# Optimization experiments

Hardware: AMD Instinct MI355X
Metric: run time of the kernel (lower is better)

The kernel has to match this reference:

```python
import jax, jax.numpy as jnp
import numpy as np
import math

D_MODEL = 768
N_HEADS = 12
B, L = 2, 2048
ALPHA = 0.3

def setup_inputs() -> dict:
    key = jax.random.key(0)
    ks = jax.random.split(key, 7)
    s = 0.02
    return {
        "x": jax.random.normal(ks[0], (B, L, D_MODEL), dtype=jnp.float32),
        "Wqkv_w": jax.random.normal(ks[1], (D_MODEL, 3 * D_MODEL), dtype=jnp.float32) * s,
        "Wqkv_b": jax.random.normal(ks[2], (3 * D_MODEL,), dtype=jnp.float32) * s,
        "sel_w": jax.random.normal(ks[3], (D_MODEL, 2), dtype=jnp.float32) * s,
        "sel_b": jax.random.normal(ks[4], (2,), dtype=jnp.float32) * s,
        "out_w": jax.random.normal(ks[5], (D_MODEL, D_MODEL), dtype=jnp.float32) * s,
        "out_b": jax.random.normal(ks[6], (D_MODEL,), dtype=jnp.float32) * s,
        "temperature": jnp.ones((1,), dtype=jnp.float32) * (math.sqrt(D_MODEL) * ALPHA),
    }

def reference(x, Wqkv_w, Wqkv_b, sel_w, sel_b, out_w, out_b, temperature):
    b, l, d = x.shape
    h = N_HEADS
    hd = d // h
    # QKV projection: (B, L, 3, H, hd)
    qkv = (x @ Wqkv_w + Wqkv_b).reshape(b, l, 3, h, hd)
    q, k_, v = qkv[:, :, 0], qkv[:, :, 1], qkv[:, :, 2]
    scale = 1.0 / math.sqrt(hd)
    scores = jnp.einsum('bthd,bshd->bhts', q, k_ * scale)  # (B,H,L,L)
    causal_mask = jnp.triu(jnp.full((l, l), -10000.0, dtype=scores.dtype), 1)
    attn = jax.nn.softmax(scores + causal_mask, axis=-1)
    ctx = jnp.einsum('bhts,bshd->bthd', attn, v).reshape(b, l, d)
    attn_output = ctx @ out_w + out_b  # (B,L,D)
    # selection gate: softmax over 2 logits, keep prob of class 1 -> (B,L,1)
    selection = jax.nn.softmax((x @ sel_w + sel_b) / temperature, axis=-1)[..., 1:]
    # eval-mode top-k routing
    k_sel = int(math.ceil(math.sqrt(l)))
    _, idx = jax.lax.top_k(selection[..., 0], k_sel)  # (B, k)
    gated = attn_output * selection  # (B,L,D)
    src = jnp.take_along_axis(gated, idx[..., None], axis=1)  # (B,k,D)
    y = jax.vmap(lambda xb, ib, sb: xb.at[ib].add(sb))(x, idx, src)
    return y
```

## Files before the change

### kernel.cpp

```cpp
#include <hip/hip_runtime.h>
#include <hip/hip_bf16.h>
#include <cstddef>

#define BATCH 2
#define SEQ   2048
#define DM    768
#define NH    12
#define HD    64
#define N3    2304
#define NKV   1536
#define KSEL  46
#define NROW  (BATCH*KSEL)
#define NCHUNK 32

typedef unsigned short ushort_t;
typedef __attribute__((ext_vector_type(8))) short bf16x8;
typedef __attribute__((ext_vector_type(4))) float f32x4;

__device__ __forceinline__ ushort_t f2bf(float f) {
  union { __hip_bfloat16 h; ushort_t u; } cv;
  cv.h = __float2bfloat16(f);
  return cv.u;
}
__device__ __forceinline__ float bf2f(ushort_t u) {
  union { unsigned int i; float f; } cv;
  cv.i = ((unsigned int)u) << 16;
  return cv.f;
}

#define GLD16(g, l)                                                         \
  __builtin_amdgcn_global_load_lds(                                         \
      (const __attribute__((address_space(1))) void*)(g),                   \
      (__attribute__((address_space(3))) void*)(l), 16, 0, 0)

__global__ __launch_bounds__(256) void prep_kernel(
    const float* __restrict__ x, const float* __restrict__ W,
    const float* __restrict__ Wo,
    const float* __restrict__ sel_w, const float* __restrict__ sel_b,
    const float* __restrict__ temp,
    ushort_t* __restrict__ xb, ushort_t* __restrict__ Wt,
    ushort_t* __restrict__ WoT,
    float* __restrict__ sel, float* __restrict__ y) {
  const int bx = blockIdx.x;
  const int tid = threadIdx.x;
  if (bx < 3072) {
    int i = bx * 256 + tid;
    float4 f = ((const float4*)x)[i];
    ushort4 o;
    o.x = f2bf(f.x); o.y = f2bf(f.y); o.z = f2bf(f.z); o.w = f2bf(f.w);
    ((ushort4*)xb)[i] = o;
  } else if (bx < 4800) {
    __shared__ float tile[32][33];
    const int bx2 = bx - 3072;
    const int n0 = (bx2 % 72) * 32, k0 = (bx2 / 72) * 32;
    const int r = tid >> 3, c4 = (tid & 7) * 4;
    float4 f = *(const float4*)&W[(size_t)(k0 + r) * N3 + n0 + c4];
    tile[r][c4] = f.x; tile[r][c4 + 1] = f.y; tile[r][c4 + 2] = f.z; tile[r][c4 + 3] = f.w;
    __syncthreads();
    ushort4 o;
    o.x = f2bf(tile[c4 + 0][r]);
    o.y = f2bf(tile[c4 + 1][r]);
    o.z = f2bf(tile[c4 + 2][r]);
    o.w = f2bf(tile[c4 + 3][r]);
    *(ushort4*)&Wt[(size_t)(n0 + r) * DM + k0 + c4] = o;
  } else if (bx < 5376) {
    __shared__ float tile2[32][33];
    const int bx3 = bx - 4800;
    const int n0 = (bx3 % 24) * 32, k0 = (bx3 / 24) * 32;
    const int r = tid >> 3, c4 = (tid & 7) * 4;
    float4 f = *(const float4*)&Wo[(size_t)(k0 + r) * DM + n0 + c4];
    tile2[r][c4] = f.x; tile2[r][c4 + 1] = f.y; tile2[r][c4 + 2] = f.z; tile2[r][c4 + 3] = f.w;
    __syncthreads();
    ushort4 o;
    o.x = f2bf(tile2[c4 + 0][r]);
    o.y = f2bf(tile2[c4 + 1][r]);
    o.z = f2bf(tile2[c4 + 2][r]);
    o.w = f2bf(tile2[c4 + 3][r]);
    *(ushort4*)&WoT[(size_t)(n0 + r) * DM + k0 + c4] = o;
  } else if (bx < 6400) {
    int wave = tid >> 6, lane = tid & 63;
    int row = (bx - 5376) * 4 + wave;
    const float* xr = x + (size_t)row * DM;
    float a0 = 0.f, a1 = 0.f;
    for (int i = 0; i < DM / 64; ++i) {
      int k = lane + 64 * i;
      float xv = xr[k];
      a0 += xv * sel_w[2 * k];
      a1 += xv * sel_w[2 * k + 1];
    }
    for (int off = 32; off; off >>= 1) {
      a0 += __shfl_xor(a0, off);
      a1 += __shfl_xor(a1, off);
    }
    if (lane == 0) {
      float t = temp[0];
      float l0 = (a0 + sel_b[0]) / t;
      float l1 = (a1 + sel_b[1]) / t;
      sel[row] = 1.0f / (1.0f + expf(l0 - l1));
    }
  } else {
    int i = (bx - 6400) * 256 + tid;
    ((float4*)y)[i] = ((const float4*)x)[i];
  }
}

__global__ __launch_bounds__(256) void topk_kernel(
    const float* __restrict__ sel, int* __restrict__ idx,
    int* __restrict__ idxp) {
  __shared__ unsigned int hist[256];
  __shared__ unsigned int cum[256];
  __shared__ int sh_b;
  __shared__ int c_gt, c_eq;
  __shared__ int tmp_gt[KSEL];
  __shared__ int eqlist[256];
  const int b = blockIdx.x, tid = threadIdx.x;

  unsigned int key[8];
  int  kidx[8];
#pragma unroll
  for (int e = 0; e < 8; ++e) {
    int i = e * 256 + tid;
    kidx[e] = i;
    key[e] = __float_as_uint(sel[b * SEQ + i]);
  }
  unsigned int prefix = 0, mask = 0;
  int r = KSEL;
#pragma unroll
  for (int p = 3; p >= 0; --p) {
    const int shift = 8 * p;
    hist[tid] = 0;
    __syncthreads();
#pragma unroll
    for (int e = 0; e < 8; ++e)
      if ((key[e] & mask) == prefix)
        atomicAdd(&hist[(key[e] >> shift) & 255], 1u);
    __syncthreads();
    cum[tid] = hist[tid];
    __syncthreads();
    for (int d = 1; d < 256; d <<= 1) {
      unsigned int t = (tid + d < 256) ? cum[tid + d] : 0;
      __syncthreads();
      cum[tid] += t;
      __syncthreads();
    }
    if (cum[tid] >= (unsigned int)r && (tid == 255 || cum[tid + 1] < (unsigned int)r))
      sh_b = tid;
    __syncthreads();
    const int bsel = sh_b;
    r -= (bsel == 255) ? 0 : (int)cum[bsel + 1];
    prefix |= ((unsigned int)bsel) << shift;
    mask |= 0xFFu << shift;
    __syncthreads();
  }
  if (tid == 0) { c_gt = 0; c_eq = 0; }
  __syncthreads();
#pragma unroll
  for (int e = 0; e < 8; ++e) {
    if (key[e] > prefix) {
      int pos = atomicAdd(&c_gt, 1);
      tmp_gt[pos] = kidx[e];
    } else if (key[e] == prefix) {
      int pos = atomicAdd(&c_eq, 1);
      if (pos < 256) eqlist[pos] = kidx[e];
    }
  }
  __syncthreads();
  if (tid == 0) {
    const int need = KSEL - c_gt;
    const int ec = (c_eq < 256) ? c_eq : 256;
    for (int a = 0; a < need; ++a) {
      int mb = a;
      for (int bb = a + 1; bb < ec; ++bb)
        if (eqlist[bb] < eqlist[mb]) mb = bb;
      int tv = eqlist[a]; eqlist[a] = eqlist[mb]; eqlist[mb] = tv;
    }
  }
  __syncthreads();
  if (tid < 64) {
    if (tid < KSEL) {
      int t = (tid < c_gt) ? tmp_gt[tid] : eqlist[tid - c_gt];
      idx[b * KSEL + tid] = t;
      idxp[b * 64 + tid] = t;
    } else {
      idxp[b * 64 + tid] = 0;
    }
  }
}

__global__ __launch_bounds__(256) void gemm_kernel(
    const ushort_t* __restrict__ Xbf,
    const ushort_t* __restrict__ Wt,
    const float* __restrict__ bias,
    const int* __restrict__ idxp,
    ushort_t* __restrict__ Ckv,
    ushort_t* __restrict__ qb) {
  __shared__ ushort_t As[128 * 32];
  __shared__ ushort_t Bs[128 * 32];
  const int bid = blockIdx.x;
  const int tid = threadIdx.x;
  const int lane = tid & 63, w = tid >> 6;
  const int wr = w >> 1, wc = w & 1;
  const int quad = lane >> 4, l16 = lane & 15;
  const int ci0 = tid;
  const int ci1 = 256 + tid;
  const bool isQ = (bid >= 384);
  int m0, n0;
  size_t ga0, ga1;
  if (isQ) {
    m0 = 0;
    n0 = (bid - 384) * 128;
    const int r0 = ci0 >> 2, r1 = ci1 >> 2;
    ga0 = (size_t)((r0 >> 6) * SEQ + idxp[r0]) * DM;
    ga1 = (size_t)((r1 >> 6) * SEQ + idxp[r1]) * DM;
  } else {
    m0 = (bid / 12) * 128;
    n0 = 768 + (bid % 12) * 128;
    ga0 = (size_t)(m0 + (ci0 >> 2)) * DM;
    ga1 = (size_t)(m0 + (ci1 >> 2)) * DM;
  }
  const size_t gb0 = (size_t)(n0 + (ci0 >> 2)) * DM;
  const size_t gb1 = (size_t)(n0 + (ci1 >> 2)) * DM;
  const int ka0 = (ci0 & 3) * 8, ka1 = (ci1 & 3) * 8;

  f32x4 acc[4][4] = {};
  for (int k0 = 0; k0 < DM; k0 += 32) {
    GLD16(Xbf + ga0 + k0 + ka0, &As[(w * 64) * 8]);
    GLD16(Xbf + ga1 + k0 + ka1, &As[(256 + w * 64) * 8]);
    GLD16(Wt + gb0 + k0 + ka0, &Bs[(w * 64) * 8]);
    GLD16(Wt + gb1 + k0 + ka1, &Bs[(256 + w * 64) * 8]);
    __syncthreads();
    bf16x8 af[4], bfr[4];
#pragma unroll
    for (int i = 0; i < 4; ++i)
      af[i] = *(const bf16x8*)&As[(wr * 64 + i * 16 + l16) * 32 + quad * 8];
#pragma unroll
    for (int j = 0; j < 4; ++j)
      bfr[j] = *(const bf16x8*)&Bs[(wc * 64 + j * 16 + l16) * 32 + quad * 8];
#pragma unroll
    for (int i = 0; i < 4; ++i)
#pragma unroll
      for (int j = 0; j < 4; ++j)
        acc[i][j] = __builtin_amdgcn_mfma_f32_16x16x32_bf16(af[i], bfr[j], acc[i][j], 0, 0, 0);
    __syncthreads();
  }
#pragma unroll
  for (int i = 0; i < 4; ++i) {
    const int row_base = wr * 64 + i * 16 + quad * 4;
#pragma unroll
    for (int j = 0; j < 4; ++j) {
      const int col = n0 + wc * 64 + j * 16 + l16;
      const float bv = bias[col];
      if (isQ) {
#pragma unroll
        for (int r = 0; r < 4; ++r)
          qb[(size_t)(row_base + r) * DM + col] = f2bf(acc[i][j][r] + bv);
      } else {
#pragma unroll
        for (int r = 0; r < 4; ++r)
          Ckv[(size_t)(m0 + row_base + r) * NKV + (col - 768)] = f2bf(acc[i][j][r] + bv);
      }
    }
  }
}

__global__ __launch_bounds__(256) void attn_chunk_kernel(
    const ushort_t* __restrict__ kv,
    const ushort_t* __restrict__ qb,
    const int* __restrict__ idx,
    float* __restrict__ m_part, float* __restrict__ l_part,
    ushort_t* __restrict__ o_part) {
  __shared__ __align__(16) ushort_t Vt[64][72];
  __shared__ __align__(16) ushort_t Ps[4][16][72];
  __shared__ int tS[64];
  __shared__ int tmaxS;
  const int tid = threadIdx.x;
  const int c = blockIdx.x, h = blockIdx.y, b = blockIdx.z;
  const int c0 = c * 64;
  if (tid < 64) {
    int t = (tid < KSEL) ? idx[b * KSEL + tid] : -1;
    tS[tid] = t;
    int tm = t;
    for (int off = 32; off; off >>= 1) tm = max(tm, __shfl_xor(tm, off));
    if (tid == 0) tmaxS = tm;
  }
  __syncthreads();
  if (c0 > tmaxS) return;

  {
    const int key = tid >> 2, ds0 = (tid & 3) * 16;
    const ushort_t* vsrc = kv + (size_t)(b * SEQ + c0 + key) * NKV + DM + h * HD + ds0;
    ushort_t tmp[16];
    *(uint4*)&tmp[0] = *(const uint4*)&vsrc[0];
    *(uint4*)&tmp[8] = *(const uint4*)&vsrc[8];
#pragma unroll
    for (int i = 0; i < 16; ++i) Vt[ds0 + i][key] = tmp[i];
  }

  const int lane = tid & 63, w = tid >> 6;
  const int quad = lane >> 4, l16 = lane & 15;

  const ushort_t* qsrc = qb + (size_t)(b * 64 + w * 16 + l16) * DM + h * HD + quad * 8;
  bf16x8 aq0 = *(const bf16x8*)&qsrc[0];
  bf16x8 aq1 = *(const bf16x8*)&qsrc[32];

  f32x4 acc[4] = {};
#pragma unroll
  for (int nt = 0; nt < 4; ++nt) {
    const ushort_t* ksrc = kv + (size_t)(b * SEQ + c0 + nt * 16 + l16) * NKV + h * HD + quad * 8;
    bf16x8 bk0 = *(const bf16x8*)&ksrc[0];
    bf16x8 bk1 = *(const bf16x8*)&ksrc[32];
    acc[nt] = __builtin_amdgcn_mfma_f32_16x16x32_bf16(aq0, bk0, acc[nt], 0, 0, 0);
    acc[nt] = __builtin_amdgcn_mfma_f32_16x16x32_bf16(aq1, bk1, acc[nt], 0, 0, 0);
  }

  float p[4][4];
  float mrow[4], lrow[4];
#pragma unroll
  for (int r = 0; r < 4; ++r) {
    const int q = w * 16 + quad * 4 + r;
    const int t = tS[q];
    float mx = -1e30f;
#pragma unroll
    for (int nt = 0; nt < 4; ++nt) {
      float s = acc[nt][r] * 0.125f;
      if (c0 + nt * 16 + l16 > t) s = -1e30f;
      p[nt][r] = s;
      mx = fmaxf(mx, s);
    }
#pragma unroll
    for (int off = 1; off < 16; off <<= 1) mx = fmaxf(mx, __shfl_xor(mx, off));
    float sum = 0.f;
#pragma unroll
    for (int nt = 0; nt < 4; ++nt) {
      float pv = __expf(p[nt][r] - mx);
      p[nt][r] = pv;
      sum += pv;
    }
#pragma unroll
    for (int off = 1; off < 16; off <<= 1) sum += __shfl_xor(sum, off);
    mrow[r] = mx; lrow[r] = sum;
  }

  const size_t pbase = ((size_t)(b * NH + h) * NCHUNK + c) * 64;
  if (l16 == 0) {
#pragma unroll
    for (int r = 0; r < 4; ++r) {
      const int q = w * 16 + quad * 4 + r;
      m_part[pbase + q] = mrow[r];
      l_part[pbase + q] = lrow[r];
    }
  }

#pragma unroll
  for (int r = 0; r < 4; ++r)
#pragma unroll
    for (int nt = 0; nt < 4; ++nt)
      Ps[w][quad * 4 + r][nt * 16 + l16] = f2bf(p[nt][r]);
  __syncthreads();

  bf16x8 ap0 = *(const bf16x8*)&Ps[w][l16][quad * 8];
  bf16x8 ap1 = *(const bf16x8*)&Ps[w][l16][32 + quad * 8];
  f32x4 acc2[4] = {};
#pragma unroll
  for (int nt = 0; nt < 4; ++nt) {
    bf16x8 bv0 = *(const bf16x8*)&Vt[nt * 16 + l16][quad * 8];
    bf16x8 bv1 = *(const bf16x8*)&Vt[nt * 16 + l16][32 + quad * 8];
    acc2[nt] = __builtin_amdgcn_mfma_f32_16x16x32_bf16(ap0, bv0, acc2[nt], 0, 0, 0);
    acc2[nt] = __builtin_amdgcn_mfma_f32_16x16x32_bf16(ap1, bv1, acc2[nt], 0, 0, 0);
  }
  ushort_t* obp = o_part + pbase * 64;
#pragma unroll
  for (int nt = 0; nt < 4; ++nt)
#pragma unroll
    for (int r = 0; r < 4; ++r)
      obp[(w * 16 + quad * 4 + r) * 64 + nt * 16 + l16] = f2bf(acc2[nt][r]);
}

__global__ __launch_bounds__(256) void attn_combine_kernel(
    const float* __restrict__ m_part, const float* __restrict__ l_part,
    const ushort_t* __restrict__ o_part, const int* __restrict__ idx,
    ushort_t* __restrict__ ctx_bf) {
  __shared__ float wgt[NCHUNK][16];
  __shared__ float linv[16];
  __shared__ int ncS[16];
  const int rg = blockIdx.x, h = blockIdx.y, b = blockIdx.z;
  const int tid = threadIdx.x;
  const size_t base = (size_t)(b * NH + h) * NCHUNK * 64;
  if (tid < 16) {
    const int q = rg * 16 + tid;
    float L = 0.f; int nc = 0;
    if (q < KSEL) {
      const int t = idx[b * KSEL + q];
      nc = (t >> 6) + 1;
      float M = -1e30f;
      for (int cc = 0; cc < nc; ++cc)
        M = fmaxf(M, m_part[base + cc * 64 + q]);
      for (int cc = 0; cc < nc; ++cc) {
        float wv = __expf(m_part[base + cc * 64 + q] - M);
        wgt[cc][tid] = wv;
        L += wv * l_part[base + cc * 64 + q];
      }
    }
    ncS[tid] = nc;
    linv[tid] = (L > 0.f) ? 1.0f / L : 0.f;
  }
  __syncthreads();
  const int rl = tid >> 4;
  const int d4 = (tid & 15) * 4;
  const int q = rg * 16 + rl;
  if (q >= KSEL) return;
  const int nc = ncS[rl];
  float4 a = {0.f, 0.f, 0.f, 0.f};
  const ushort_t* obp = o_part + base * 64 + (size_t)q * 64 + d4;
  for (int cc = 0; cc < nc; ++cc) {
    const float wv = wgt[cc][rl];
    const ushort4 ov = *(const ushort4*)&obp[(size_t)cc * 4096];
    a.x += wv * bf2f(ov.x); a.y += wv * bf2f(ov.y);
    a.z += wv * bf2f(ov.z); a.w += wv * bf2f(ov.w);
  }
  const float li = linv[rl];
  ushort4 o;
  o.x = f2bf(a.x * li); o.y = f2bf(a.y * li);
  o.z = f2bf(a.z * li); o.w = f2bf(a.w * li);
  *(ushort4*)&ctx_bf[(size_t)(b * 64 + q) * DM + h * HD + d4] = o;
}

__global__ __launch_bounds__(256) void outproj_kernel(
    const ushort_t* __restrict__ ctx_bf,
    const ushort_t* __restrict__ WoT,
    const float* __restrict__ ob, const int* __restrict__ idx,
    const float* __restrict__ sel, float* __restrict__ y) {
  __shared__ ushort_t As[128 * 32];
  __shared__ ushort_t Bs[128 * 32];
  const int tid = threadIdx.x;
  const int lane = tid & 63, w = tid >> 6;
  const int wr = w >> 1, wc = w & 1;
  const int n0 = blockIdx.x * 128;
  const int quad = lane >> 4, l16 = lane & 15;
  const int ci0 = tid;
  const int ci1 = 256 + tid;
  const size_t ga0 = (size_t)(ci0 >> 2) * DM;
  const size_t ga1 = (size_t)(ci1 >> 2) * DM;
  const size_t gb0 = (size_t)(n0 + (ci0 >> 2)) * DM;
  const size_t gb1 = (size_t)(n0 + (ci1 >> 2)) * DM;
  const int ka0 = (ci0 & 3) * 8, ka1 = (ci1 & 3) * 8;
  f32x4 acc[4][4] = {};
  for (int k0 = 0; k0 < DM; k0 += 32) {
    GLD16(ctx_bf + ga0 + k0 + ka0, &As[(w * 64) * 8]);
    GLD16(ctx_bf + ga1 + k0 + ka1, &As[(256 + w * 64) * 8]);
    GLD16(WoT + gb0 + k0 + ka0, &Bs[(w * 64) * 8]);
    GLD16(WoT + gb1 + k0 + ka1, &Bs[(256 + w * 64) * 8]);
    __syncthreads();
    bf16x8 af[4], bfr[4];
#pragma unroll
    for (int i = 0; i < 4; ++i)
      af[i] = *(const bf16x8*)&As[(wr * 64 + i * 16 + l16) * 32 + quad * 8];
#pragma unroll
    for (int j = 0; j < 4; ++j)
      bfr[j] = *(const bf16x8*)&Bs[(wc * 64 + j * 16 + l16) * 32 + quad * 8];
#pragma unroll
    for (int i = 0; i < 4; ++i)
#pragma unroll
      for (int j = 0; j < 4; ++j)
        acc[i][j] = __builtin_amdgcn_mfma_f32_16x16x32_bf16(af[i], bfr[j], acc[i][j], 0, 0, 0);
    __syncthreads();
  }
#pragma unroll
  for (int i = 0; i < 4; ++i) {
#pragma unroll
    for (int r = 0; r < 4; ++r) {
      const int row = wr * 64 + i * 16 + quad * 4 + r;
      const int b = row >> 6, jj = row & 63;
      if (jj >= KSEL) continue;
      const int t = idx[b * KSEL + jj];
      const float sv = sel[b * SEQ + t];
      float* yr = y + (size_t)(b * SEQ + t) * DM;
#pragma unroll
      for (int j = 0; j < 4; ++j) {
        const int col = n0 + wc * 64 + j * 16 + l16;
        yr[col] += (acc[i][j][r] + ob[col]) * sv;
      }
    }
  }
}

extern "C" void kernel_launch(void* const* d_in, const int* in_sizes, int n_in,
                              void* d_out, int out_size, void* d_ws, size_t ws_size,
                              hipStream_t stream) {
  const float* x      = (const float*)d_in[0];
  const float* Wqkv_w = (const float*)d_in[1];
  const float* Wqkv_b = (const float*)d_in[2];
  const float* sel_w  = (const float*)d_in[3];
  const float* sel_b  = (const float*)d_in[4];
  const float* out_w  = (const float*)d_in[5];
  const float* out_b  = (const float*)d_in[6];
  const float* temp   = (const float*)d_in[7];
  float* y = (float*)d_out;

  char* wsb = (char*)d_ws;
  ushort_t* kv     = (ushort_t*)wsb;  wsb += (size_t)BATCH * SEQ * NKV * 2;
  ushort_t* o_part = (ushort_t*)wsb;  wsb += (size_t)24 * NCHUNK * 64 * 64 * 2;
  float*    m_part = (float*)wsb;     wsb += (size_t)24 * NCHUNK * 64 * 4;
  float*    l_part = (float*)wsb;     wsb += (size_t)24 * NCHUNK * 64 * 4;
  float*    sel    = (float*)wsb;     wsb += (size_t)BATCH * SEQ * 4;
  int*      idx    = (int*)wsb;       wsb += 128 * 4;
  int*      idxp   = (int*)wsb;       wsb += 128 * 4;
  ushort_t* ctx_bf = (ushort_t*)wsb;  wsb += (size_t)128 * DM * 2;
  ushort_t* qb     = (ushort_t*)wsb;  wsb += (size_t)128 * DM * 2;
  ushort_t* Xbf    = (ushort_t*)wsb;  wsb += (size_t)BATCH * SEQ * DM * 2;
  ushort_t* Wt     = (ushort_t*)wsb;  wsb += (size_t)N3 * DM * 2;
  ushort_t* WoT    = (ushort_t*)wsb;  wsb += (size_t)DM * DM * 2;

  prep_kernel<<<dim3(9472), 256, 0, stream>>>(x, Wqkv_w, out_w, sel_w, sel_b, temp,
                                              Xbf, Wt, WoT, sel, y);
  topk_kernel<<<dim3(BATCH), 256, 0, stream>>>(sel, idx, idxp);
  gemm_kernel<<<dim3(390), 256, 0, stream>>>(Xbf, Wt, Wqkv_b, idxp, kv, qb);
  attn_chunk_kernel<<<dim3(NCHUNK, NH, BATCH), 256, 0, stream>>>(kv, qb, idx, m_part, l_part, o_part);
  attn_combine_kernel<<<dim3(3, NH, BATCH), 256, 0, stream>>>(m_part, l_part, o_part, idx, ctx_bf);
  outproj_kernel<<<dim3(6), 256, 0, stream>>>(ctx_bf, WoT, out_b, idx, sel, y);
}
```

Measured before the change: 160.4 us.

## Fuse prep passes, sort top-k indices descending, skip inactive attention waves, split-K outproj

Merges the x-to-bf16 conversion, the copy of x into y and the selection-gate dot product into one pass per row, so x is read once instead of three times. Top-k indices are now sorted in descending position order. The attention chunk kernel can then exit early by comparing against the first index, and it skips whole waves whose queries all precede the chunk. The output projection is split in two along K across 12 blocks and accumulates with atomics, adding parallelism at the cost of atomic traffic and nondeterministic float summation order.

```diff
diff --git a/kernel.cpp b/kernel.cpp
--- a/kernel.cpp
+++ b/kernel.cpp
@@ -43,15 +43,39 @@
     float* __restrict__ sel, float* __restrict__ y) {
   const int bx = blockIdx.x;
   const int tid = threadIdx.x;
-  if (bx < 3072) {
-    int i = bx * 256 + tid;
-    float4 f = ((const float4*)x)[i];
-    ushort4 o;
-    o.x = f2bf(f.x); o.y = f2bf(f.y); o.z = f2bf(f.z); o.w = f2bf(f.w);
-    ((ushort4*)xb)[i] = o;
-  } else if (bx < 4800) {
+  if (bx < 4096) {
+    __shared__ float s0[4], s1[4];
+    const int r = bx;
+    const int wv = tid >> 6, lane = tid & 63;
+    float a0 = 0.f, a1 = 0.f;
+    if (tid < 192) {
+      const int i = r * 192 + tid;
+      const float4 f = ((const float4*)x)[i];
+      ((float4*)y)[i] = f;
+      ushort4 o;
+      o.x = f2bf(f.x); o.y = f2bf(f.y); o.z = f2bf(f.z); o.w = f2bf(f.w);
+      ((ushort4*)xb)[i] = o;
+      const int k = tid * 4;
+      a0 = f.x * sel_w[2*k] + f.y * sel_w[2*k+2] + f.z * sel_w[2*k+4] + f.w * sel_w[2*k+6];
+      a1 = f.x * sel_w[2*k+1] + f.y * sel_w[2*k+3] + f.z * sel_w[2*k+5] + f.w * sel_w[2*k+7];
+    }
+    for (int off = 32; off; off >>= 1) {
+      a0 += __shfl_xor(a0, off);
+      a1 += __shfl_xor(a1, off);
+    }
+    if (lane == 0) { s0[wv] = a0; s1[wv] = a1; }
+    __syncthreads();
+    if (tid == 0) {
+      float b0 = s0[0] + s0[1] + s0[2] + s0[3];
+      float b1 = s1[0] + s1[1] + s1[2] + s1[3];
+      float t = temp[0];
+      float l0 = (b0 + sel_b[0]) / t;
+      float l1 = (b1 + sel_b[1]) / t;
+      sel[r] = 1.0f / (1.0f + expf(l0 - l1));
+    }
+  } else if (bx < 5824) {
     __shared__ float tile[32][33];
-    const int bx2 = bx - 3072;
+    const int bx2 = bx - 4096;
     const int n0 = (bx2 % 72) * 32, k0 = (bx2 / 72) * 32;
     const int r = tid >> 3, c4 = (tid & 7) * 4;
     float4 f = *(const float4*)&W[(size_t)(k0 + r) * N3 + n0 + c4];
@@ -63,9 +87,9 @@
     o.z = f2bf(tile[c4 + 2][r]);
     o.w = f2bf(tile[c4 + 3][r]);
     *(ushort4*)&Wt[(size_t)(n0 + r) * DM + k0 + c4] = o;
-  } else if (bx < 5376) {
+  } else {
     __shared__ float tile2[32][33];
-    const int bx3 = bx - 4800;
+    const int bx3 = bx - 5824;
     const int n0 = (bx3 % 24) * 32, k0 = (bx3 / 24) * 32;
     const int r = tid >> 3, c4 = (tid & 7) * 4;
     float4 f = *(const float4*)&Wo[(size_t)(k0 + r) * DM + n0 + c4];
@@ -77,30 +101,6 @@
     o.z = f2bf(tile2[c4 + 2][r]);
     o.w = f2bf(tile2[c4 + 3][r]);
     *(ushort4*)&WoT[(size_t)(n0 + r) * DM + k0 + c4] = o;
-  } else if (bx < 6400) {
-    int wave = tid >> 6, lane = tid & 63;
-    int row = (bx - 5376) * 4 + wave;
-    const float* xr = x + (size_t)row * DM;
-    float a0 = 0.f, a1 = 0.f;
-    for (int i = 0; i < DM / 64; ++i) {
-      int k = lane + 64 * i;
-      float xv = xr[k];
-      a0 += xv * sel_w[2 * k];
-      a1 += xv * sel_w[2 * k + 1];
-    }
-    for (int off = 32; off; off >>= 1) {
-      a0 += __shfl_xor(a0, off);
-      a1 += __shfl_xor(a1, off);
-    }
-    if (lane == 0) {
-      float t = temp[0];
-      float l0 = (a0 + sel_b[0]) / t;
-      float l1 = (a1 + sel_b[1]) / t;
-      sel[row] = 1.0f / (1.0f + expf(l0 - l1));
-    }
-  } else {
-    int i = (bx - 6400) * 256 + tid;
-    ((float4*)y)[i] = ((const float4*)x)[i];
   }
 }
 
@@ -113,6 +113,7 @@
   __shared__ int c_gt, c_eq;
   __shared__ int tmp_gt[KSEL];
   __shared__ int eqlist[256];
+  __shared__ int win[KSEL];
   const int b = blockIdx.x, tid = threadIdx.x;
 
   unsigned int key[8];
@@ -176,15 +177,17 @@
     }
   }
   __syncthreads();
-  if (tid < 64) {
-    if (tid < KSEL) {
-      int t = (tid < c_gt) ? tmp_gt[tid] : eqlist[tid - c_gt];
-      idx[b * KSEL + tid] = t;
-      idxp[b * 64 + tid] = t;
-    } else {
-      idxp[b * 64 + tid] = 0;
-    }
-  }
+  if (tid < KSEL)
+    win[tid] = (tid < c_gt) ? tmp_gt[tid] : eqlist[tid - c_gt];
+  __syncthreads();
+  if (tid < KSEL) {
+    const int t = win[tid];
+    int rank = 0;
+    for (int u = 0; u < KSEL; ++u) rank += (win[u] > t);
+    idx[b * KSEL + rank] = t;
+    idxp[b * 64 + rank] = t;
+  }
+  if (tid >= KSEL && tid < 64) idxp[b * 64 + tid] = 0;
 }
 
 __global__ __launch_bounds__(256) void gemm_kernel(
@@ -272,19 +275,17 @@
   __shared__ __align__(16) ushort_t Vt[64][72];
   __shared__ __align__(16) ushort_t Ps[4][16][72];
   __shared__ int tS[64];
-  __shared__ int tmaxS;
   const int tid = threadIdx.x;
   const int c = blockIdx.x, h = blockIdx.y, b = blockIdx.z;
   const int c0 = c * 64;
-  if (tid < 64) {
-    int t = (tid < KSEL) ? idx[b * KSEL + tid] : -1;
-    tS[tid] = t;
-    int tm = t;
-    for (int off = 32; off; off >>= 1) tm = max(tm, __shfl_xor(tm, off));
-    if (tid == 0) tmaxS = tm;
-  }
-  __syncthreads();
-  if (c0 > tmaxS) return;
+  if (tid < 64)
+    tS[tid] = (tid < KSEL) ? idx[b * KSEL + tid] : -1;
+  __syncthreads();
+  if (c0 > tS[0]) return;
+
+  const int lane = tid & 63, w = tid >> 6;
+  const int quad = lane >> 4, l16 = lane & 15;
+  const bool wave_active = (tS[w * 16] >= c0);
 
   {
     const int key = tid >> 2, ds0 = (tid & 3) * 16;
@@ -296,67 +297,66 @@
     for (int i = 0; i < 16; ++i) Vt[ds0 + i][key] = tmp[i];
   }
 
-  const int lane = tid & 63, w = tid >> 6;
-  const int quad = lane >> 4, l16 = lane & 15;
-
-  const ushort_t* qsrc = qb + (size_t)(b * 64 + w * 16 + l16) * DM + h * HD + quad * 8;
-  bf16x8 aq0 = *(const bf16x8*)&qsrc[0];
-  bf16x8 aq1 = *(const bf16x8*)&qsrc[32];
-
-  f32x4 acc[4] = {};
-#pragma unroll
-  for (int nt = 0; nt < 4; ++nt) {
-    const ushort_t* ksrc = kv + (size_t)(b * SEQ + c0 + nt * 16 + l16) * NKV + h * HD + quad * 8;
-    bf16x8 bk0 = *(const bf16x8*)&ksrc[0];
-    bf16x8 bk1 = *(const bf16x8*)&ksrc[32];
-    acc[nt] = __builtin_amdgcn_mfma_f32_16x16x32_bf16(aq0, bk0, acc[nt], 0, 0, 0);
-    acc[nt] = __builtin_amdgcn_mfma_f32_16x16x32_bf16(aq1, bk1, acc[nt], 0, 0, 0);
-  }
-
-  float p[4][4];
-  float mrow[4], lrow[4];
-#pragma unroll
-  for (int r = 0; r < 4; ++r) {
-    const int q = w * 16 + quad * 4 + r;
-    const int t = tS[q];
-    float mx = -1e30f;
+  const size_t pbase = ((size_t)(b * NH + h) * NCHUNK + c) * 64;
+  if (wave_active) {
+    const ushort_t* qsrc = qb + (size_t)(b * 64 + w * 16 + l16) * DM + h * HD + quad * 8;
+    bf16x8 aq0 = *(const bf16x8*)&qsrc[0];
+    bf16x8 aq1 = *(const bf16x8*)&qsrc[32];
+
+    f32x4 acc[4] = {};
 #pragma unroll
     for (int nt = 0; nt < 4; ++nt) {
-      float s = acc[nt][r] * 0.125f;
-      if (c0 + nt * 16 + l16 > t) s = -1e30f;
-      p[nt][r] = s;
-      mx = fmaxf(mx, s);
-    }
-#pragma unroll
-    for (int off = 1; off < 16; off <<= 1) mx = fmaxf(mx, __shfl_xor(mx, off));
-    float sum = 0.f;
-#pragma unroll
-    for (int nt = 0; nt < 4; ++nt) {
-      float pv = __expf(p[nt][r] - mx);
-      p[nt][r] = pv;
-      sum += pv;
-    }
-#pragma unroll
-    for (int off = 1; off < 16; off <<= 1) sum += __shfl_xor(sum, off);
-    mrow[r] = mx; lrow[r] = sum;
-  }
-
-  const size_t pbase = ((size_t)(b * NH + h) * NCHUNK + c) * 64;
-  if (l16 == 0) {
+      const ushort_t* ksrc = kv + (size_t)(b * SEQ + c0 + nt * 16 + l16) * NKV + h * HD + quad * 8;
+      bf16x8 bk0 = *(const bf16x8*)&ksrc[0];
+      bf16x8 bk1 = *(const bf16x8*)&ksrc[32];
+      acc[nt] = __builtin_amdgcn_mfma_f32_16x16x32_bf16(aq0, bk0, acc[nt], 0, 0, 0);
+      acc[nt] = __builtin_amdgcn_mfma_f32_16x16x32_bf16(aq1, bk1, acc[nt], 0, 0, 0);
+    }
+
+    float p[4][4];
+    float mrow[4], lrow[4];
 #pragma unroll
     for (int r = 0; r < 4; ++r) {
       const int q = w * 16 + quad * 4 + r;
-      m_part[pbase + q] = mrow[r];
-      l_part[pbase + q] = lrow[r];
-    }
-  }
-
-#pragma unroll
-  for (int r = 0; r < 4; ++r)
-#pragma unroll
-    for (int nt = 0; nt < 4; ++nt)
-      Ps[w][quad * 4 + r][nt * 16 + l16] = f2bf(p[nt][r]);
-  __syncthreads();
+      const int t = tS[q];
+      float mx = -1e30f;
+#pragma unroll
+      for (int nt = 0; nt < 4; ++nt) {
+        float s = acc[nt][r] * 0.125f;
+        if (c0 + nt * 16 + l16 > t) s = -1e30f;
+        p[nt][r] = s;
+        mx = fmaxf(mx, s);
+      }
+#pragma unroll
+      for (int off = 1; off < 16; off <<= 1) mx = fmaxf(mx, __shfl_xor(mx, off));
+      float sum = 0.f;
+#pragma unroll
+      for (int nt = 0; nt < 4; ++nt) {
+        float pv = __expf(p[nt][r] - mx);
+        p[nt][r] = pv;
+        sum += pv;
+      }
+#pragma unroll
+      for (int off = 1; off < 16; off <<= 1) sum += __shfl_xor(sum, off);
+      mrow[r] = mx; lrow[r] = sum;
+    }
+
+    if (l16 == 0) {
+#pragma unroll
+      for (int r = 0; r < 4; ++r) {
+        const int q = w * 16 + quad * 4 + r;
+        m_part[pbase + q] = mrow[r];
+        l_part[pbase + q] = lrow[r];
+      }
+    }
+#pragma unroll
+    for (int r = 0; r < 4; ++r)
+#pragma unroll
+      for (int nt = 0; nt < 4; ++nt)
+        Ps[w][quad * 4 + r][nt * 16 + l16] = f2bf(p[nt][r]);
+  }
+  __syncthreads();
+  if (!wave_active) return;
 
   bf16x8 ap0 = *(const bf16x8*)&Ps[w][l16][quad * 8];
   bf16x8 ap1 = *(const bf16x8*)&Ps[w][l16][32 + quad * 8];
@@ -435,7 +435,8 @@
   const int tid = threadIdx.x;
   const int lane = tid & 63, w = tid >> 6;
   const int wr = w >> 1, wc = w & 1;
-  const int n0 = blockIdx.x * 128;
+  const int n0 = (blockIdx.x % 6) * 128;
+  const int kh = blockIdx.x / 6;
   const int quad = lane >> 4, l16 = lane & 15;
   const int ci0 = tid;
   const int ci1 = 256 + tid;
@@ -445,7 +446,7 @@
   const size_t gb1 = (size_t)(n0 + (ci1 >> 2)) * DM;
   const int ka0 = (ci0 & 3) * 8, ka1 = (ci1 & 3) * 8;
   f32x4 acc[4][4] = {};
-  for (int k0 = 0; k0 < DM; k0 += 32) {
+  for (int k0 = kh * 384; k0 < kh * 384 + 384; k0 += 32) {
     GLD16(ctx_bf + ga0 + k0 + ka0, &As[(w * 64) * 8]);
     GLD16(ctx_bf + ga1 + k0 + ka1, &As[(256 + w * 64) * 8]);
     GLD16(WoT + gb0 + k0 + ka0, &Bs[(w * 64) * 8]);
@@ -478,7 +479,8 @@
 #pragma unroll
       for (int j = 0; j < 4; ++j) {
         const int col = n0 + wc * 64 + j * 16 + l16;
-        yr[col] += (acc[i][j][r] + ob[col]) * sv;
+        const float val = (acc[i][j][r] + (kh == 0 ? ob[col] : 0.f)) * sv;
+        atomicAdd(&yr[col], val);
       }
     }
   }
@@ -511,11 +513,11 @@
   ushort_t* Wt     = (ushort_t*)wsb;  wsb += (size_t)N3 * DM * 2;
   ushort_t* WoT    = (ushort_t*)wsb;  wsb += (size_t)DM * DM * 2;
 
-  prep_kernel<<<dim3(9472), 256, 0, stream>>>(x, Wqkv_w, out_w, sel_w, sel_b, temp,
+  prep_kernel<<<dim3(6400), 256, 0, stream>>>(x, Wqkv_w, out_w, sel_w, sel_b, temp,
                                               Xbf, Wt, WoT, sel, y);
   topk_kernel<<<dim3(BATCH), 256, 0, stream>>>(sel, idx, idxp);
   gemm_kernel<<<dim3(390), 256, 0, stream>>>(Xbf, Wt, Wqkv_b, idxp, kv, qb);
   attn_chunk_kernel<<<dim3(NCHUNK, NH, BATCH), 256, 0, stream>>>(kv, qb, idx, m_part, l_part, o_part);
   attn_combine_kernel<<<dim3(3, NH, BATCH), 256, 0, stream>>>(m_part, l_part, o_part, idx, ctx_bf);
-  outproj_kernel<<<dim3(6), 256, 0, stream>>>(ctx_bf, WoT, out_b, idx, sel, y);
-}
+  outproj_kernel<<<dim3(12), 256, 0, stream>>>(ctx_bf, WoT, out_b, idx, sel, y);
+}
```

Result: slower. 165.8 us (+3.4%).
